# Performance work log

Measured on AMD Instinct MI355X. Metric: run time of the kernel, lower is better.

## Reference

```python
import jax, jax.numpy as jnp
from jax import lax
import numpy as np
import math


def make_kernel():
    # StyleGAN2 blur kernel [1,3,3,1], normalized outer product
    k = jnp.array([1.0, 3.0, 3.0, 1.0], dtype=jnp.float32)
    k2 = jnp.outer(k, k)
    return k2 / jnp.sum(k2)


def upfirdn2d(x, kernel, up=1, pad=(0, 0)):
    # x: [B,C,H,W]; depthwise FIR filter, optional zero-insert upsampling
    C = x.shape[1]
    w = jnp.tile(jnp.flip(kernel)[None, None].astype(x.dtype), (C, 1, 1, 1))
    # torch upfirdn pads up-1 trailing zeros after the last sample; lhs_dilation
    # only inserts zeros between samples, so fold the extra zeros into pad[1].
    p = (pad[0], pad[1] + up - 1)
    return lax.conv_general_dilated(
        x, w, (1, 1), (p, p), lhs_dilation=(up, up), feature_group_count=C)


def modulated_conv(x, weight, style, demodulate=True, up=False):
    # per-sample weight modulation + demodulation, executed as grouped conv
    B, Cin, H, W = x.shape
    Cout, _, k, _ = weight.shape
    scale = 1.0 / math.sqrt(Cin * k * k)
    w = scale * weight[None] * style[:, None, :, None, None]  # [B,Cout,Cin,k,k]
    if demodulate:
        d = lax.rsqrt(jnp.sum(w * w, axis=(2, 3, 4)) + 1e-8)
        w = w * d[:, :, None, None, None]
    xg = x.reshape(1, B * Cin, H, W)
    if up:
        # conv_transpose2d(stride=2, pad=0) == lhs-dilated conv with flipped kernel
        wg = jnp.flip(w, (-2, -1)).reshape(B * Cout, Cin, k, k)
        out = lax.conv_general_dilated(
            xg, wg, (1, 1), ((k - 1, k - 1), (k - 1, k - 1)),
            lhs_dilation=(2, 2), feature_group_count=B)
    else:
        pad = k // 2
        out = lax.conv_general_dilated(
            xg, w.reshape(B * Cout, Cin, k, k), (1, 1),
            ((pad, pad), (pad, pad)), feature_group_count=B)
    return out.reshape(B, Cout, out.shape[2], out.shape[3])


def fused_lrelu(x, bias):
    y = x + bias[None, :, None, None]
    return jnp.where(y >= 0, y, 0.2 * y) * math.sqrt(2.0)


def setup_inputs() -> dict:
    key = jax.random.key(0)
    ks = jax.random.split(key, 12)
    B, C, H = 8, 512, 32
    f = jnp.float32
    return {
        "x": jax.random.normal(ks[0], (B, C, H, H), f),
        "skip": jax.random.normal(ks[1], (B, 3, H, H), f),
        "w1": jax.random.normal(ks[2], (C, C, 3, 3), f),
        "b1": jnp.zeros((C,), f),
        "s1": jax.random.normal(ks[3], (B, C), f),
        "nw1": jax.random.normal(ks[4], (1,), f) * 0.1,
        "n1": jax.random.normal(ks[5], (B, 1, 2 * H, 2 * H), f),
        "w2": jax.random.normal(ks[6], (C, C, 3, 3), f),
        "b2": jnp.zeros((C,), f),
        "s2": jax.random.normal(ks[7], (B, C), f),
        "nw2": jax.random.normal(ks[8], (1,), f) * 0.1,
        "n2": jax.random.normal(ks[9], (B, 1, 2 * H, 2 * H), f),
        "w_rgb": jax.random.normal(ks[10], (3, C, 1, 1), f),
        "b_rgb": jnp.zeros((3,), f),
        "s_rgb": jax.random.normal(ks[11], (B, C), f),
    }


def reference(x, skip, w1, b1, s1, nw1, n1, w2, b2, s2, nw2, n2,
              w_rgb, b_rgb, s_rgb):
    kern = make_kernel()
    # conv1: upsampling modulated conv + blur (Blur with upsample_factor=2)
    out = modulated_conv(x, w1, s1, demodulate=True, up=True)
    out = upfirdn2d(out, kern * 4.0, up=1, pad=(1, 1))
    out = out + nw1 * n1          # NoiseInjection
    out = fused_lrelu(out, b1)    # FusedLeakyReLU
    # conv2: plain modulated conv
    out = modulated_conv(out, w2, s2, demodulate=True)
    out = out + nw2 * n2
    out = fused_lrelu(out, b2)
    # ToRGB: 1x1 mod conv, no demodulation, + bias; skip = rgb + upsample(skip)
    rgb = modulated_conv(out, w_rgb, s_rgb, demodulate=False)
    rgb = rgb + b_rgb[None, :, None, None]
    skip_up = upfirdn2d(skip, kern * 4.0, up=2, pad=(2, 1))
    return rgb + skip_up
```

## Files before the change

### kernel.cpp

```cpp
#include <hip/hip_runtime.h>
#include <stdint.h>

typedef unsigned short ushort_t;
typedef unsigned int uint_t;
typedef __bf16 bf16x8 __attribute__((ext_vector_type(8)));
typedef float f32x4 __attribute__((ext_vector_type(4)));

#define GLOBAL_AS __attribute__((address_space(1)))
#define LDS_AS    __attribute__((address_space(3)))

#define SCALE_CONV 0.014731391f
#define SCALE_RGB  0.044194174f
#define SQRT2_F    1.41421356237f

__device__ __forceinline__ void async_cp16(const void* g, void* l) {
  __builtin_amdgcn_global_load_lds((const GLOBAL_AS uint_t*)g,
                                   (LDS_AS uint_t*)l, 16, 0, 0);
}
__device__ __forceinline__ ushort_t f2bf(float v) {
  union { float f; uint_t u; } c; c.f = v;
  uint_t r = c.u + 0x7fffu + ((c.u >> 16) & 1u);
  return (ushort_t)(r >> 16);
}
__device__ __forceinline__ float bf2f(ushort_t u) {
  union { uint_t u; float f; } c; c.u = ((uint_t)u) << 16;
  return c.f;
}

__global__ __launch_bounds__(256) void prep_all(
    const float* __restrict__ x, const float* __restrict__ s1,
    ushort_t* __restrict__ xpad,
    const float* __restrict__ w1, const float* __restrict__ w2,
    ushort_t* __restrict__ wt1, ushort_t* __restrict__ wt2,
    float* __restrict__ wsqT1, float* __restrict__ wsqT2) {
  if (blockIdx.x < 256) {
    __shared__ ushort_t t[32 * 520];
    const int b  = blockIdx.x >> 5;
    const int j1 = blockIdx.x & 31;
    for (int idx = threadIdx.x; idx < 512 * 32; idx += 256) {
      int ci = idx >> 5, j2 = idx & 31;
      float v = x[(size_t)(b * 512 + ci) * 1024 + j1 * 32 + j2];
      v *= s1[b * 512 + ci] * SCALE_CONV;
      t[j2 * 520 + ci] = f2bf(v);
    }
    __syncthreads();
    for (int idx = threadIdx.x; idx < 32 * 512; idx += 256) {
      int j2 = idx >> 9, ci = idx & 511;
      xpad[((size_t)(b * 34 + j1 + 1) * 34 + (j2 + 1)) * 512 + ci] = t[j2 * 520 + ci];
    }
    return;
  }
  int t = (blockIdx.x - 256) * 256 + threadIdx.x;
  const float* w  = (t < 262144) ? w1 : w2;
  ushort_t*   wt  = (t < 262144) ? wt1 : wt2;
  float*      wq  = (t < 262144) ? wsqT1 : wsqT2;
  int tt = t & 262143;
  int ci = tt & 511, co = tt >> 9;
  const float* wp = w + (size_t)(co * 512 + ci) * 9;
  float sq = 0.f;
#pragma unroll
  for (int u = 0; u < 9; ++u) {
    float v = wp[u];
    sq += v * v;
    wt[((size_t)u * 512 + co) * 512 + ci] = f2bf(v);
  }
  wq[ci * 512 + co] = sq;
}

__global__ __launch_bounds__(256) void demod3(
    const float* __restrict__ wsqT1, const float* __restrict__ s1, float* __restrict__ d1,
    const float* __restrict__ wsqT2, const float* __restrict__ s2, float* __restrict__ d2) {
  const float* wq = blockIdx.z ? wsqT2 : wsqT1;
  const float* s  = blockIdx.z ? s2 : s1;
  float*       d  = blockIdx.z ? d2 : d1;
  const int b   = blockIdx.y;
  const int co  = blockIdx.x * 64 + (threadIdx.x & 63);
  const int cig = threadIdx.x >> 6;
  __shared__ float ssq[512];
  __shared__ float red[4][64];
  for (int i = threadIdx.x; i < 512; i += 256) {
    float v = s[b * 512 + i];
    ssq[i] = v * v;
  }
  __syncthreads();
  float a = 0.f;
#pragma unroll 4
  for (int ci = cig * 128; ci < cig * 128 + 128; ++ci)
    a += wq[ci * 512 + co] * ssq[ci];
  red[cig][threadIdx.x & 63] = a;
  __syncthreads();
  if (cig == 0) {
    int l = threadIdx.x & 63;
    float tot = red[0][l] + red[1][l] + red[2][l] + red[3][l];
    d[b * 512 + co] = rsqrtf(tot * (1.f / 4608.f) + 1e-8f);
  }
}

__global__ __launch_bounds__(256) void border_zero(
    ushort_t* __restrict__ xpad, ushort_t* __restrict__ ypad, ushort_t* __restrict__ opad,
    float* __restrict__ rgbpart) {
  const int z = blockIdx.z;
  if (z == 3) {
    int i = (blockIdx.y * 66 + blockIdx.x) * 256 + threadIdx.x;
    if (i < 24576) {
      uint4 z4 = {0, 0, 0, 0};
      *(uint4*)(rgbpart + i * 4) = z4;
    }
    return;
  }
  ushort_t* p = (z == 0) ? xpad : (z == 1 ? ypad : opad);
  const int W = (z == 0) ? 34 : (z == 1 ? 67 : 66);
  const int nb = 4 * W - 4;
  const int t = blockIdx.x * 256 + threadIdx.x;
  const int pix = t >> 6, ch = (t & 63) * 8;
  if (pix >= nb) return;
  const int b = blockIdx.y;
  int y, x;
  if (pix < W)          { y = 0;     x = pix; }
  else if (pix < 2 * W) { y = W - 1; x = pix - W; }
  else { int q = pix - 2 * W; y = 1 + (q >> 1); x = (q & 1) ? W - 1 : 0; }
  uint4 z4 = {0, 0, 0, 0};
  *(uint4*)(p + ((size_t)(b * W + y) * W + x) * 512 + ch) = z4;
}

__constant__ int           c_ph_off[4]  = {0, 4, 6, 8};
__constant__ int           c_ph_ntap[4] = {4, 2, 2, 1};
__constant__ unsigned char c_tap_u1[9]  = {0,0,1,1, 0,1, 1,1, 1};
__constant__ unsigned char c_tap_u2[9]  = {0,1,0,1, 1,1, 0,1, 1};
__constant__ unsigned char c_tap_pl[9]  = {8,6,2,0, 7,1, 5,3, 4};

__global__ __launch_bounds__(256, 3) void gemm_conv1(
    const ushort_t* __restrict__ inp, const ushort_t* __restrict__ wt,
    const float* __restrict__ dmod, ushort_t* __restrict__ outp) {
  const int g = blockIdx.x;
  const int mtile = ((g >> 7) << 3) | (g & 7);
  if (mtile >= 69) return;
  const int sub   = (g >> 3) & 15;
  const int a     = sub >> 2;
  const int ntile = sub & 3;
  const int a1 = a >> 1, a2 = a & 1;

  __shared__ ushort_t ldsA[128 * 64];
  __shared__ ushort_t ldsB[128 * 64];

  const int tid  = threadIdx.x;
  const int lane = tid & 63;
  const int wv   = tid >> 6;
  const int wm   = wv & 1;
  const int wn   = wv >> 1;
  const int l16  = lane & 15;
  const int quad = lane >> 4;

  const int cl = ((lane & 7) - (lane >> 3)) & 7;
  const char* pA[4];
  const char* pB[4];
#pragma unroll
  for (int t = 0; t < 4; ++t) {
    int row = wv * 32 + t * 8 + (lane >> 3);
    int m   = mtile * 128 + row;
    if (m > 8711) m = 8711;
    int b = m / 1089, rr = m % 1089;
    int p1 = rr / 33, p2 = rr % 33;
    size_t pix = ((size_t)(b * 34 + p1) * 34 + p2) * 512;
    pA[t] = (const char*)inp + pix * 2 + cl * 16;
    int n = ntile * 128 + row;
    pB[t] = (const char*)wt + (size_t)n * 1024 + cl * 16;
  }
  char* dstA[4];
  char* dstB[4];
#pragma unroll
  for (int t = 0; t < 4; ++t) {
    dstA[t] = (char*)ldsA + wv * 4096 + t * 1024;
    dstB[t] = (char*)ldsB + wv * 4096 + t * 1024;
  }

  int offA[4], offB[4];
#pragma unroll
  for (int i = 0; i < 4; ++i) {
    int r  = wm * 64 + i * 16 + l16;
    int rn = wn * 64 + i * 16 + l16;
    offA[i] = r  * 64 + (((quad + r)  & 7) << 3);
    offB[i] = rn * 64 + (((quad + rn) & 7) << 3);
  }

  f32x4 acc[4][4];
#pragma unroll
  for (int i = 0; i < 4; ++i)
#pragma unroll
    for (int j = 0; j < 4; ++j) acc[i][j] = (f32x4){0.f, 0.f, 0.f, 0.f};

  const int ntap = c_ph_ntap[a];
#pragma unroll 1
  for (int ti = 0; ti < ntap; ++ti) {
    int e = c_ph_off[a] + ti;
    int aoff = ((int)c_tap_u1[e] * 34 + (int)c_tap_u2[e]) * 1024;
    int boff = (int)c_tap_pl[e] * 524288;
#pragma unroll 1
    for (int kc = 0; kc < 8; ++kc) {
      const int koff = kc * 128;
      __syncthreads();
#pragma unroll
      for (int t = 0; t < 4; ++t) async_cp16(pA[t] + aoff + koff, dstA[t]);
#pragma unroll
      for (int t = 0; t < 4; ++t) async_cp16(pB[t] + boff + koff, dstB[t]);
      __syncthreads();
#pragma unroll
      for (int kk = 0; kk < 2; ++kk) {
        const int kx = kk << 5;
        bf16x8 af[4], bg[4];
#pragma unroll
        for (int i = 0; i < 4; ++i) af[i] = *reinterpret_cast<const bf16x8*>(ldsA + (offA[i] ^ kx));
#pragma unroll
        for (int j = 0; j < 4; ++j) bg[j] = *reinterpret_cast<const bf16x8*>(ldsB + (offB[j] ^ kx));
#pragma unroll
        for (int i = 0; i < 4; ++i)
#pragma unroll
          for (int j = 0; j < 4; ++j)
            acc[i][j] = __builtin_amdgcn_mfma_f32_16x16x32_bf16(af[i], bg[j], acc[i][j], 0, 0, 0);
      }
    }
  }

  int co_[4];
#pragma unroll
  for (int j = 0; j < 4; ++j) co_[j] = ntile * 128 + wn * 64 + j * 16 + l16;

#pragma unroll
  for (int i = 0; i < 4; ++i) {
#pragma unroll
    for (int r = 0; r < 4; ++r) {
      int m = mtile * 128 + wm * 64 + i * 16 + quad * 4 + r;
      if (m < 8712) {
        int b = m / 1089, rr = m % 1089;
        int p1 = rr / 33, p2 = rr % 33;
        if ((a1 == 0 || p1 < 32) && (a2 == 0 || p2 < 32)) {
          int o1 = 2 * p1 + a1, o2 = 2 * p2 + a2;
          size_t ob = ((size_t)(b * 67 + o1 + 1) * 67 + (o2 + 1)) * 512;
#pragma unroll
          for (int j = 0; j < 4; ++j)
            outp[ob + co_[j]] = f2bf(acc[i][j][r] * dmod[b * 512 + co_[j]]);
        }
      }
    }
  }
}

__global__ __launch_bounds__(256, 3) void gemm_conv2(
    const ushort_t* __restrict__ inp, const ushort_t* __restrict__ wt,
    const float* __restrict__ dmod, const float* __restrict__ noise,
    const float* __restrict__ nw, const float* __restrict__ bias,
    const float* __restrict__ srgb, const float* __restrict__ wrgb,
    float* __restrict__ rgbpart) {
  const int g = blockIdx.x;
  const int mtile = ((g >> 5) << 3) | (g & 7);
  const int ntile = (g >> 3) & 3;

  __shared__ ushort_t ldsA[128 * 64];
  __shared__ ushort_t ldsB[128 * 64];

  const int tid  = threadIdx.x;
  const int lane = tid & 63;
  const int wv   = tid >> 6;
  const int wm   = wv & 1;
  const int wn   = wv >> 1;
  const int l16  = lane & 15;
  const int quad = lane >> 4;

  const int cl = ((lane & 7) - (lane >> 3)) & 7;
  const char* pA[4];
  const char* pB[4];
#pragma unroll
  for (int t = 0; t < 4; ++t) {
    int row = wv * 32 + t * 8 + (lane >> 3);
    int m   = mtile * 128 + row;
    int b = m >> 12, o1 = (m >> 6) & 63, o2 = m & 63;
    size_t pix = ((size_t)(b * 66 + o1 + 1) * 66 + (o2 + 1)) * 512;
    pA[t] = (const char*)inp + pix * 2 + cl * 16;
    int n = ntile * 128 + row;
    pB[t] = (const char*)wt + (size_t)n * 1024 + cl * 16;
  }
  char* dstA[4];
  char* dstB[4];
#pragma unroll
  for (int t = 0; t < 4; ++t) {
    dstA[t] = (char*)ldsA + wv * 4096 + t * 1024;
    dstB[t] = (char*)ldsB + wv * 4096 + t * 1024;
  }

  int offA[4], offB[4];
#pragma unroll
  for (int i = 0; i < 4; ++i) {
    int r  = wm * 64 + i * 16 + l16;
    int rn = wn * 64 + i * 16 + l16;
    offA[i] = r  * 64 + (((quad + r)  & 7) << 3);
    offB[i] = rn * 64 + (((quad + rn) & 7) << 3);
  }

  f32x4 acc[4][4];
#pragma unroll
  for (int i = 0; i < 4; ++i)
#pragma unroll
    for (int j = 0; j < 4; ++j) acc[i][j] = (f32x4){0.f, 0.f, 0.f, 0.f};

#pragma unroll 1
  for (int ti = 0; ti < 9; ++ti) {
    int aoff = ((ti / 3 - 1) * 66 + (ti % 3 - 1)) * 1024;
    int boff = ti * 524288;
#pragma unroll 1
    for (int kc = 0; kc < 8; ++kc) {
      const int koff = kc * 128;
      __syncthreads();
#pragma unroll
      for (int t = 0; t < 4; ++t) async_cp16(pA[t] + aoff + koff, dstA[t]);
#pragma unroll
      for (int t = 0; t < 4; ++t) async_cp16(pB[t] + boff + koff, dstB[t]);
      __syncthreads();
#pragma unroll
      for (int kk = 0; kk < 2; ++kk) {
        const int kx = kk << 5;
        bf16x8 af[4], bg[4];
#pragma unroll
        for (int i = 0; i < 4; ++i) af[i] = *reinterpret_cast<const bf16x8*>(ldsA + (offA[i] ^ kx));
#pragma unroll
        for (int j = 0; j < 4; ++j) bg[j] = *reinterpret_cast<const bf16x8*>(ldsB + (offB[j] ^ kx));
#pragma unroll
        for (int i = 0; i < 4; ++i)
#pragma unroll
          for (int j = 0; j < 4; ++j)
            acc[i][j] = __builtin_amdgcn_mfma_f32_16x16x32_bf16(af[i], bg[j], acc[i][j], 0, 0, 0);
      }
    }
  }

  const int b = mtile >> 5;
  int co_[4];
#pragma unroll
  for (int j = 0; j < 4; ++j) co_[j] = ntile * 128 + wn * 64 + j * 16 + l16;
  const float nwv = nw[0];
  float dj_[4], sj_[4], bj_[4], wr[3][4];
#pragma unroll
  for (int j = 0; j < 4; ++j) {
    dj_[j] = dmod[b * 512 + co_[j]];
    sj_[j] = srgb[b * 512 + co_[j]] * SCALE_RGB;
    bj_[j] = bias[co_[j]];
#pragma unroll
    for (int c = 0; c < 3; ++c) wr[c][j] = wrgb[c * 512 + co_[j]];
  }
#pragma unroll
  for (int i = 0; i < 4; ++i) {
#pragma unroll
    for (int r = 0; r < 4; ++r) {
      int m = mtile * 128 + wm * 64 + i * 16 + quad * 4 + r;
      int o1 = (m >> 6) & 63, o2 = m & 63;
      float nz = nwv * noise[(b << 12) + (o1 << 6) + o2];
      float vv[4];
#pragma unroll
      for (int j = 0; j < 4; ++j) {
        float v = acc[i][j][r] * dj_[j] + nz + bj_[j];
        v = (v >= 0.f ? v : 0.2f * v) * SQRT2_F;
        vv[j] = v * sj_[j];
      }
#pragma unroll
      for (int c = 0; c < 3; ++c) {
        float s = vv[0] * wr[c][0] + vv[1] * wr[c][1] + vv[2] * wr[c][2] + vv[3] * wr[c][3];
        s += __shfl_xor(s, 1);
        s += __shfl_xor(s, 2);
        s += __shfl_xor(s, 4);
        s += __shfl_xor(s, 8);
        if (l16 == 0) atomicAdd(&rgbpart[c * 32768 + m], s);
      }
    }
  }
}

__global__ __launch_bounds__(256) void blur_noise_act(
    const ushort_t* __restrict__ y1pad, const float* __restrict__ noise,
    const float* __restrict__ nw, const float* __restrict__ bias,
    const float* __restrict__ s2, ushort_t* __restrict__ out1pad) {
  const int cg  = threadIdx.x & 63;
  const int pg  = blockIdx.x * 4 + (threadIdx.x >> 6);
  const int b   = pg >> 9;
  const int q1  = (pg >> 3) & 63;
  const int q2g = (pg & 7) * 8;
  const float cw[4] = {0.25f, 0.75f, 0.75f, 0.25f};

  float acc[8][8];
#pragma unroll
  for (int j = 0; j < 8; ++j)
#pragma unroll
    for (int e = 0; e < 8; ++e) acc[j][e] = 0.f;

#pragma unroll
  for (int t2 = 0; t2 < 11; ++t2) {
    int cc = q2g + t2;
    float vt[8];
#pragma unroll
    for (int e = 0; e < 8; ++e) vt[e] = 0.f;
#pragma unroll
    for (int t1 = 0; t1 < 4; ++t1) {
      const ushort_t* p = y1pad + ((size_t)(b * 67 + q1 + t1) * 67 + cc) * 512 + cg * 8;
      ushort_t v[8];
      *(uint4*)v = *(const uint4*)p;
#pragma unroll
      for (int e = 0; e < 8; ++e) vt[e] += cw[t1] * bf2f(v[e]);
    }
#pragma unroll
    for (int j = 0; j < 8; ++j) {
      int t = t2 - j;
      if (t >= 0 && t < 4) {
#pragma unroll
        for (int e = 0; e < 8; ++e) acc[j][e] += cw[t] * vt[e];
      }
    }
  }

  const float nwv = nw[0];
  float bj[8], sj[8];
#pragma unroll
  for (int e = 0; e < 8; ++e) {
    bj[e] = bias[cg * 8 + e];
    sj[e] = s2[b * 512 + cg * 8 + e] * SCALE_CONV;
  }
#pragma unroll
  for (int j = 0; j < 8; ++j) {
    int q2 = q2g + j;
    float nz = nwv * noise[(b << 12) + (q1 << 6) + q2];
    ushort_t o[8];
#pragma unroll
    for (int e = 0; e < 8; ++e) {
      float v = acc[j][e] + nz + bj[e];
      v = (v >= 0.f ? v : 0.2f * v) * SQRT2_F * sj[e];
      o[e] = f2bf(v);
    }
    *(uint4*)(out1pad + ((size_t)(b * 66 + q1 + 1) * 66 + (q2 + 1)) * 512 + cg * 8) = *(uint4*)o;
  }
}

__global__ __launch_bounds__(256) void rgb_finish(
    const float* __restrict__ rgbpart, const float* __restrict__ brgb,
    const float* __restrict__ skip, float* __restrict__ out) {
  const int t = blockIdx.x * 256 + threadIdx.x;
  if (t >= 98304) return;
  const int m = t & 32767, c = t >> 15;
  const int b = m >> 12, o1 = (m >> 6) & 63, o2 = m & 63;
  int P1 = o1 >> 1, P2 = o2 >> 1;
  int jy0, jy1, jx0, jx1;
  float wy0, wy1, wx0, wx1;
  if ((o1 & 1) == 0) { jy0 = P1 - 1; wy0 = .25f; jy1 = P1;     wy1 = .75f; }
  else               { jy0 = P1;     wy0 = .75f; jy1 = P1 + 1; wy1 = .25f; }
  if ((o2 & 1) == 0) { jx0 = P2 - 1; wx0 = .25f; jx1 = P2;     wx1 = .75f; }
  else               { jx0 = P2;     wx0 = .75f; jx1 = P2 + 1; wx1 = .25f; }
  const float* sp = skip + (size_t)(b * 3 + c) * 1024;
  float sv = 0.f;
  if (jy0 >= 0 && jy0 < 32) {
    if (jx0 >= 0 && jx0 < 32) sv += wy0 * wx0 * sp[jy0 * 32 + jx0];
    if (jx1 >= 0 && jx1 < 32) sv += wy0 * wx1 * sp[jy0 * 32 + jx1];
  }
  if (jy1 >= 0 && jy1 < 32) {
    if (jx0 >= 0 && jx0 < 32) sv += wy1 * wx0 * sp[jy1 * 32 + jx0];
    if (jx1 >= 0 && jx1 < 32) sv += wy1 * wx1 * sp[jy1 * 32 + jx1];
  }
  out[((size_t)(b * 3 + c) << 12) + (o1 << 6) + o2] = rgbpart[c * 32768 + m] + brgb[c] + sv;
}

extern "C" void kernel_launch(void* const* d_in, const int* in_sizes, int n_in,
                              void* d_out, int out_size, void* d_ws, size_t ws_size,
                              hipStream_t stream) {
  const float* x    = (const float*)d_in[0];
  const float* skip = (const float*)d_in[1];
  const float* w1   = (const float*)d_in[2];
  const float* b1   = (const float*)d_in[3];
  const float* s1   = (const float*)d_in[4];
  const float* nw1  = (const float*)d_in[5];
  const float* n1   = (const float*)d_in[6];
  const float* w2   = (const float*)d_in[7];
  const float* b2   = (const float*)d_in[8];
  const float* s2   = (const float*)d_in[9];
  const float* nw2  = (const float*)d_in[10];
  const float* n2   = (const float*)d_in[11];
  const float* wrgb = (const float*)d_in[12];
  const float* brgb = (const float*)d_in[13];
  const float* srgb = (const float*)d_in[14];

  char* ws = (char*)d_ws;
  const size_t XPAD_B  = (size_t)8 * 34 * 34 * 512 * 2;
  const size_t Y1PAD_B = (size_t)8 * 67 * 67 * 512 * 2;
  const size_t OUT1_B  = (size_t)8 * 66 * 66 * 512 * 2;
  const size_t WT_B    = (size_t)9 * 512 * 512 * 2;
  size_t off = 0;
  ushort_t* xpad1   = (ushort_t*)(ws + off); off += XPAD_B;
  ushort_t* y1pad   = (ushort_t*)(ws + off); off += Y1PAD_B;
  ushort_t* out1pad = (ushort_t*)(ws + off); off += OUT1_B;
  ushort_t* wt1     = (ushort_t*)(ws + off); off += WT_B;
  ushort_t* wt2     = (ushort_t*)(ws + off); off += WT_B;
  float*    d1      = (float*)(ws + off);    off += 8 * 512 * 4;
  float*    d2      = (float*)(ws + off);    off += 8 * 512 * 4;
  float*    rgbpart = (float*)(ws + off);    off += 3 * 32768 * 4;
  float*    wsqT1  = (float*)y1pad;
  float*    wsqT2  = wsqT1 + 512 * 512;

  prep_all<<<2304, 256, 0, stream>>>(x, s1, xpad1, w1, w2, wt1, wt2, wsqT1, wsqT2);
  demod3<<<dim3(8, 8, 2), 256, 0, stream>>>(wsqT1, s1, d1, wsqT2, s2, d2);
  border_zero<<<dim3(66, 8, 4), 256, 0, stream>>>(xpad1, y1pad, out1pad, rgbpart);

  gemm_conv1<<<1152, 256, 0, stream>>>(xpad1, wt1, d1, y1pad);
  blur_noise_act<<<1024, 256, 0, stream>>>(y1pad, n1, nw1, b1, s2, out1pad);
  gemm_conv2<<<1024, 256, 0, stream>>>(
      out1pad, wt2, d2, n2, nw2, b2, srgb, wrgb, rgbpart);
  rgb_finish<<<384, 256, 0, stream>>>(rgbpart, brgb, skip, (float*)d_out);
}
```

Baseline: 375.8 us.

## Software-pipeline conv GEMM loads through registers with prefetch two steps ahead

```diff
diff --git a/kernel.cpp b/kernel.cpp
--- a/kernel.cpp
+++ b/kernel.cpp
@@ -6,17 +6,10 @@
 typedef __bf16 bf16x8 __attribute__((ext_vector_type(8)));
 typedef float f32x4 __attribute__((ext_vector_type(4)));
 
-#define GLOBAL_AS __attribute__((address_space(1)))
-#define LDS_AS    __attribute__((address_space(3)))
-
 #define SCALE_CONV 0.014731391f
 #define SCALE_RGB  0.044194174f
 #define SQRT2_F    1.41421356237f
 
-__device__ __forceinline__ void async_cp16(const void* g, void* l) {
-  __builtin_amdgcn_global_load_lds((const GLOBAL_AS uint_t*)g,
-                                   (LDS_AS uint_t*)l, 16, 0, 0);
-}
 __device__ __forceinline__ ushort_t f2bf(float v) {
   union { float f; uint_t u; } c; c.f = v;
   uint_t r = c.u + 0x7fffu + ((c.u >> 16) & 1u);
@@ -129,6 +122,106 @@
 __constant__ unsigned char c_tap_u2[9]  = {0,1,0,1, 1,1, 0,1, 1};
 __constant__ unsigned char c_tap_pl[9]  = {8,6,2,0, 7,1, 5,3, 4};
 
+template <int MODE>
+__device__ __forceinline__ void gemm_core(
+    int mtile, int ntile, int a,
+    const ushort_t* __restrict__ inp, const ushort_t* __restrict__ wt,
+    f32x4 (&acc)[4][4], int (&offA)[4], int (&offB)[4],
+    ushort_t* ldsA, ushort_t* ldsB) {
+  const int tid  = threadIdx.x;
+  const int lane = tid & 63;
+  const int wv   = tid >> 6;
+
+  const int phoff = (MODE == 0) ? c_ph_off[a] : 0;
+  const int nk    = (MODE == 0) ? c_ph_ntap[a] * 8 : 72;
+
+  const int cl = ((lane & 7) - (lane >> 3)) & 7;
+  const char* pA[4];
+  const char* pB[4];
+#pragma unroll
+  for (int t = 0; t < 4; ++t) {
+    int row = wv * 32 + t * 8 + (lane >> 3);
+    int m   = mtile * 128 + row;
+    size_t pix;
+    if (MODE == 0) {
+      if (m > 8711) m = 8711;
+      int b = m / 1089, rr = m % 1089;
+      int p1 = rr / 33, p2 = rr % 33;
+      pix = ((size_t)(b * 34 + p1) * 34 + p2) * 512;
+    } else {
+      int b = m >> 12, o1 = (m >> 6) & 63, o2 = m & 63;
+      pix = ((size_t)(b * 66 + o1 + 1) * 66 + (o2 + 1)) * 512;
+    }
+    pA[t] = (const char*)inp + pix * 2 + cl * 16;
+    int n = ntile * 128 + row;
+    pB[t] = (const char*)wt + (size_t)n * 1024 + cl * 16;
+  }
+  ushort_t* dstA[4];
+  ushort_t* dstB[4];
+#pragma unroll
+  for (int t = 0; t < 4; ++t) {
+    dstA[t] = ldsA + wv * 2048 + t * 512 + lane * 8;
+    dstB[t] = ldsB + wv * 2048 + t * 512 + lane * 8;
+  }
+
+  uint4 rA[4], rB[4];
+  auto loadRegs = [&](int kn) {
+    int tap = kn >> 3, kc = kn & 7;
+    int aoff, boff;
+    if (MODE == 0) {
+      int e = phoff + tap;
+      aoff = ((int)c_tap_u1[e] * 34 + (int)c_tap_u2[e]) * 1024 + kc * 128;
+      boff = (int)c_tap_pl[e] * 524288 + kc * 128;
+    } else {
+      int ty = (tap * 86) >> 8;
+      int tx = tap - ty * 3;
+      aoff = ((ty - 1) * 66 + (tx - 1)) * 1024 + kc * 128;
+      boff = tap * 524288 + kc * 128;
+    }
+#pragma unroll
+    for (int t = 0; t < 4; ++t) {
+      rA[t] = *(const uint4*)(pA[t] + aoff);
+      rB[t] = *(const uint4*)(pB[t] + boff);
+    }
+  };
+  auto writeLds = [&]() {
+#pragma unroll
+    for (int t = 0; t < 4; ++t) {
+      *(uint4*)dstA[t] = rA[t];
+      *(uint4*)dstB[t] = rB[t];
+    }
+  };
+
+  loadRegs(0);
+  writeLds();
+  if (nk > 1) loadRegs(1);
+  asm volatile("s_waitcnt lgkmcnt(0)\ns_barrier" ::: "memory");
+
+#pragma unroll 1
+  for (int k = 0; k < nk; ++k) {
+#pragma unroll
+    for (int kk = 0; kk < 2; ++kk) {
+      const int kx = kk << 5;
+      bf16x8 af[4], bg[4];
+#pragma unroll
+      for (int i = 0; i < 4; ++i) af[i] = *reinterpret_cast<const bf16x8*>(ldsA + (offA[i] ^ kx));
+#pragma unroll
+      for (int j = 0; j < 4; ++j) bg[j] = *reinterpret_cast<const bf16x8*>(ldsB + (offB[j] ^ kx));
+#pragma unroll
+      for (int i = 0; i < 4; ++i)
+#pragma unroll
+        for (int j = 0; j < 4; ++j)
+          acc[i][j] = __builtin_amdgcn_mfma_f32_16x16x32_bf16(af[i], bg[j], acc[i][j], 0, 0, 0);
+    }
+    if (k + 1 < nk) {
+      asm volatile("s_waitcnt lgkmcnt(0)\ns_barrier" ::: "memory");
+      writeLds();
+      if (k + 2 < nk) loadRegs(k + 2);
+      asm volatile("s_waitcnt lgkmcnt(0)\ns_barrier" ::: "memory");
+    }
+  }
+}
+
 __global__ __launch_bounds__(256, 3) void gemm_conv1(
     const ushort_t* __restrict__ inp, const ushort_t* __restrict__ wt,
     const float* __restrict__ dmod, ushort_t* __restrict__ outp) {
@@ -143,36 +236,12 @@
   __shared__ ushort_t ldsA[128 * 64];
   __shared__ ushort_t ldsB[128 * 64];
 
-  const int tid  = threadIdx.x;
-  const int lane = tid & 63;
-  const int wv   = tid >> 6;
+  const int lane = threadIdx.x & 63;
+  const int wv   = threadIdx.x >> 6;
   const int wm   = wv & 1;
   const int wn   = wv >> 1;
   const int l16  = lane & 15;
   const int quad = lane >> 4;
-
-  const int cl = ((lane & 7) - (lane >> 3)) & 7;
-  const char* pA[4];
-  const char* pB[4];
-#pragma unroll
-  for (int t = 0; t < 4; ++t) {
-    int row = wv * 32 + t * 8 + (lane >> 3);
-    int m   = mtile * 128 + row;
-    if (m > 8711) m = 8711;
-    int b = m / 1089, rr = m % 1089;
-    int p1 = rr / 33, p2 = rr % 33;
-    size_t pix = ((size_t)(b * 34 + p1) * 34 + p2) * 512;
-    pA[t] = (const char*)inp + pix * 2 + cl * 16;
-    int n = ntile * 128 + row;
-    pB[t] = (const char*)wt + (size_t)n * 1024 + cl * 16;
-  }
-  char* dstA[4];
-  char* dstB[4];
-#pragma unroll
-  for (int t = 0; t < 4; ++t) {
-    dstA[t] = (char*)ldsA + wv * 4096 + t * 1024;
-    dstB[t] = (char*)ldsB + wv * 4096 + t * 1024;
-  }
 
   int offA[4], offB[4];
 #pragma unroll
@@ -182,49 +251,17 @@
     offA[i] = r  * 64 + (((quad + r)  & 7) << 3);
     offB[i] = rn * 64 + (((quad + rn) & 7) << 3);
   }
-
   f32x4 acc[4][4];
 #pragma unroll
   for (int i = 0; i < 4; ++i)
 #pragma unroll
     for (int j = 0; j < 4; ++j) acc[i][j] = (f32x4){0.f, 0.f, 0.f, 0.f};
 
-  const int ntap = c_ph_ntap[a];
-#pragma unroll 1
-  for (int ti = 0; ti < ntap; ++ti) {
-    int e = c_ph_off[a] + ti;
-    int aoff = ((int)c_tap_u1[e] * 34 + (int)c_tap_u2[e]) * 1024;
-    int boff = (int)c_tap_pl[e] * 524288;
-#pragma unroll 1
-    for (int kc = 0; kc < 8; ++kc) {
-      const int koff = kc * 128;
-      __syncthreads();
-#pragma unroll
-      for (int t = 0; t < 4; ++t) async_cp16(pA[t] + aoff + koff, dstA[t]);
-#pragma unroll
-      for (int t = 0; t < 4; ++t) async_cp16(pB[t] + boff + koff, dstB[t]);
-      __syncthreads();
-#pragma unroll
-      for (int kk = 0; kk < 2; ++kk) {
-        const int kx = kk << 5;
-        bf16x8 af[4], bg[4];
-#pragma unroll
-        for (int i = 0; i < 4; ++i) af[i] = *reinterpret_cast<const bf16x8*>(ldsA + (offA[i] ^ kx));
-#pragma unroll
-        for (int j = 0; j < 4; ++j) bg[j] = *reinterpret_cast<const bf16x8*>(ldsB + (offB[j] ^ kx));
-#pragma unroll
-        for (int i = 0; i < 4; ++i)
-#pragma unroll
-          for (int j = 0; j < 4; ++j)
-            acc[i][j] = __builtin_amdgcn_mfma_f32_16x16x32_bf16(af[i], bg[j], acc[i][j], 0, 0, 0);
-      }
-    }
-  }
+  gemm_core<0>(mtile, ntile, a, inp, wt, acc, offA, offB, ldsA, ldsB);
 
   int co_[4];
 #pragma unroll
   for (int j = 0; j < 4; ++j) co_[j] = ntile * 128 + wn * 64 + j * 16 + l16;
-
 #pragma unroll
   for (int i = 0; i < 4; ++i) {
 #pragma unroll
@@ -258,34 +295,12 @@
   __shared__ ushort_t ldsA[128 * 64];
   __shared__ ushort_t ldsB[128 * 64];
 
-  const int tid  = threadIdx.x;
-  const int lane = tid & 63;
-  const int wv   = tid >> 6;
+  const int lane = threadIdx.x & 63;
+  const int wv   = threadIdx.x >> 6;
   const int wm   = wv & 1;
   const int wn   = wv >> 1;
   const int l16  = lane & 15;
   const int quad = lane >> 4;
-
-  const int cl = ((lane & 7) - (lane >> 3)) & 7;
-  const char* pA[4];
-  const char* pB[4];
-#pragma unroll
-  for (int t = 0; t < 4; ++t) {
-    int row = wv * 32 + t * 8 + (lane >> 3);
-    int m   = mtile * 128 + row;
-    int b = m >> 12, o1 = (m >> 6) & 63, o2 = m & 63;
-    size_t pix = ((size_t)(b * 66 + o1 + 1) * 66 + (o2 + 1)) * 512;
-    pA[t] = (const char*)inp + pix * 2 + cl * 16;
-    int n = ntile * 128 + row;
-    pB[t] = (const char*)wt + (size_t)n * 1024 + cl * 16;
-  }
-  char* dstA[4];
-  char* dstB[4];
-#pragma unroll
-  for (int t = 0; t < 4; ++t) {
-    dstA[t] = (char*)ldsA + wv * 4096 + t * 1024;
-    dstB[t] = (char*)ldsB + wv * 4096 + t * 1024;
-  }
 
   int offA[4], offB[4];
 #pragma unroll
@@ -295,42 +310,13 @@
     offA[i] = r  * 64 + (((quad + r)  & 7) << 3);
     offB[i] = rn * 64 + (((quad + rn) & 7) << 3);
   }
-
   f32x4 acc[4][4];
 #pragma unroll
   for (int i = 0; i < 4; ++i)
 #pragma unroll
     for (int j = 0; j < 4; ++j) acc[i][j] = (f32x4){0.f, 0.f, 0.f, 0.f};
 
-#pragma unroll 1
-  for (int ti = 0; ti < 9; ++ti) {
-    int aoff = ((ti / 3 - 1) * 66 + (ti % 3 - 1)) * 1024;
-    int boff = ti * 524288;
-#pragma unroll 1
-    for (int kc = 0; kc < 8; ++kc) {
-      const int koff = kc * 128;
-      __syncthreads();
-#pragma unroll
-      for (int t = 0; t < 4; ++t) async_cp16(pA[t] + aoff + koff, dstA[t]);
-#pragma unroll
-      for (int t = 0; t < 4; ++t) async_cp16(pB[t] + boff + koff, dstB[t]);
-      __syncthreads();
-#pragma unroll
-      for (int kk = 0; kk < 2; ++kk) {
-        const int kx = kk << 5;
-        bf16x8 af[4], bg[4];
-#pragma unroll
-        for (int i = 0; i < 4; ++i) af[i] = *reinterpret_cast<const bf16x8*>(ldsA + (offA[i] ^ kx));
-#pragma unroll
-        for (int j = 0; j < 4; ++j) bg[j] = *reinterpret_cast<const bf16x8*>(ldsB + (offB[j] ^ kx));
-#pragma unroll
-        for (int i = 0; i < 4; ++i)
-#pragma unroll
-          for (int j = 0; j < 4; ++j)
-            acc[i][j] = __builtin_amdgcn_mfma_f32_16x16x32_bf16(af[i], bg[j], acc[i][j], 0, 0, 0);
-      }
-    }
-  }
+  gemm_core<1>(mtile, ntile, 0, inp, wt, acc, offA, offB, ldsA, ldsB);
 
   const int b = mtile >> 5;
   int co_[4];
```

Measured after the change: 1.116 ms. 197% more time.
